# Kernel optimization log

Hardware: AMD Instinct MI355X
Metric: run time of the kernel (lower is better)

## Reference

```python
import jax, jax.numpy as jnp
import numpy as np

NUM_HEAD = 8
HEAD_DIM = 32
MAX_DIST = 128
RATIO = 4  # smooth_embedding_ratio


def setup_inputs() -> dict:
    key = jax.random.key(0)
    ks = jax.random.split(key, 8)
    B, L, C = 4, 2048, 64
    H, D, md = NUM_HEAD, HEAD_DIM, MAX_DIST
    Wsm = (2 * md + 1) // RATIO  # 64

    def g(k, shape, scale=0.05):
        return jax.random.normal(k, shape, dtype=jnp.float32) * scale

    return {
        "x": g(ks[0], (B, L, C), 1.0),
        "Wq": g(ks[1], (C, H * D)),
        "bq": jnp.zeros((H * D,), jnp.float32),
        "Wk": g(ks[2], (C, H * D)),
        "bk": jnp.zeros((H * D,), jnp.float32),
        "Wv": g(ks[3], (C, H)),
        "distance_pe": g(ks[4], (H, D, Wsm, 1)),
        "u_pe": g(ks[5], (H, 1, 1, D)),
        "v_pe": g(ks[6], (H, 1, 1, D)),
    }


def reference(x, Wq, bq, Wk, bk, Wv, distance_pe, u_pe, v_pe):
    H, D, md = NUM_HEAD, HEAD_DIM, MAX_DIST
    W = 2 * md + 1
    B, L, _ = x.shape

    # projections, split into heads: (H, B, L, D)
    q = (x @ Wq + bq).reshape(B, L, H, D).transpose(2, 0, 1, 3)
    k = (x @ Wk + bk).reshape(B, L, H, D).transpose(2, 0, 1, 3)
    v = jax.nn.sigmoid(x @ Wv).transpose(2, 0, 1)  # (H, B, L)

    # Banded (q+u) @ k^T without materializing the full LxL score matrix.
    # TF does matmul + diag_part(k=(-md, md)) + permute + double reverse, which
    # equals att[h,b,n,m] = <q_u[h,b,(L-1-n)-(m-md)], k[h,b,L-1-n]> (0 if OOB).
    q_u = q + u_pe  # (H, B, L, D)
    q_pad = jnp.pad(q_u, ((0, 0), (0, 0), (md, md), (0, 0)))  # zeros match diag_part padding

    def band_at(m):
        # q_pad[j + 2*md - m] == q_u[j - (m - md)] (zero when out of range)
        qs = jax.lax.dynamic_slice_in_dim(q_pad, 2 * md - m, L, axis=2)
        return jnp.einsum('hbld,hbld->hbl', qs, k)

    band = jax.lax.map(band_at, jnp.arange(W))  # (W, H, B, L)
    att = jnp.transpose(band, (1, 2, 3, 0))[:, :, ::-1, :]  # (H, B, L, W)

    # Smoothed distance PE: bilinear upsample width Wsm -> W (TF2 half-pixel centers)
    smooth_pe = jax.image.resize(distance_pe, (H, D, W, 1), method='linear')[..., 0]  # (H, D, W)
    att = att + jnp.einsum('hbld,hdw->hblw', q + v_pe, smooth_pe)

    att = jax.nn.softmax(att * (float(D) ** -0.5), axis=-1)
    att = att * v[..., None]  # sigmoid value gating

    out = att.sum(axis=2)  # global mode: reduce over data_length -> (H, B, W)
    return jnp.transpose(out, (1, 2, 0))  # (B, W, H)
```

## Files before the change

kernel.cpp:

```cpp
#include <hip/hip_runtime.h>
#include <math.h>

#define NH 8
#define HD 32
#define MD 128
#define NW 257
#define NWP 272
#define WSM 64
#define NB 4
#define NL 2048
#define NC 64
#define NHD 256
#define SP 40
#define ROWS 128
#define WIN 384
#define SC2 0.2550928063161107f

#define PM_BLK 512
#define VV_BLK 64
#define SPE_BLK 34
#define WTS 72

using bf16x8 = __attribute__((ext_vector_type(8))) short;
using f32x4  = __attribute__((ext_vector_type(4))) float;
using i32x4  = __attribute__((ext_vector_type(4))) int;

__device__ __forceinline__ unsigned cvtpk(float lo, float hi) {
  unsigned r;
  asm("v_cvt_pk_bf16_f32 %0, %1, %2" : "=v"(r) : "v"(lo), "v"(hi));
  return r;
}
__device__ __forceinline__ void stb(unsigned short* p, float f) {
  *p = (unsigned short)cvtpk(f, f);
}

__global__ __launch_bounds__(256, 4) void projmm_kernel(
    const float* __restrict__ x,
    const float* __restrict__ Wq, const float* __restrict__ bq,
    const float* __restrict__ Wk, const float* __restrict__ bk,
    const float* __restrict__ Wv, const float* __restrict__ dpe,
    const float* __restrict__ u_pe, const float* __restrict__ v_pe,
    unsigned short* __restrict__ qu, unsigned short* __restrict__ qv,
    unsigned short* __restrict__ kb, float* __restrict__ vv,
    unsigned short* __restrict__ spt, float* __restrict__ out) {
  __shared__ __align__(16) unsigned short wt[128 * WTS];
  const int t = threadIdx.x;
  const int bid = blockIdx.x;

  if (bid >= PM_BLK + VV_BLK) {
    const int base = (bid - PM_BLK - VV_BLK) * 256 + t;
    if (base < NB * NW * NH) out[base] = 0.f;
    for (int idx = base; idx < NH * NWP * HD; idx += SPE_BLK * 256) {
      const int d = idx & 31;
      const int hm = idx >> 5;
      const int m = hm % NWP;
      const int h = hm / NWP;
      float val = 0.f;
      if (m < NW) {
        float tt = (m + 0.5f) * ((float)WSM / (float)NW) - 0.5f;
        tt = fminf(fmaxf(tt, 0.f), (float)(WSM - 1));
        const int i0 = (int)tt;
        const float f = tt - (float)i0;
        const int i1 = (i0 + 1 < WSM) ? i0 + 1 : WSM - 1;
        const float* bse = dpe + ((size_t)h * HD + d) * WSM;
        val = (bse[i0] * (1.f - f) + bse[i1] * f) * SC2;
      }
      stb(spt + idx, val);
    }
    return;
  }

  if (bid >= PM_BLK) {
    const int row = (bid - PM_BLK) * 128 + (t >> 1);
    const int h0 = (t & 1) * 4;
    const float* xr = x + (size_t)row * NC;
    float a0 = 0.f, a1 = 0.f, a2 = 0.f, a3 = 0.f;
#pragma unroll
    for (int c4 = 0; c4 < NC / 4; ++c4) {
      const float4 xv = *reinterpret_cast<const float4*>(xr + 4 * c4);
#pragma unroll
      for (int j = 0; j < 4; ++j) {
        const float xs = j == 0 ? xv.x : j == 1 ? xv.y : j == 2 ? xv.z : xv.w;
        const float4 wv = *reinterpret_cast<const float4*>(Wv + (4 * c4 + j) * NH + h0);
        a0 = fmaf(xs, wv.x, a0);
        a1 = fmaf(xs, wv.y, a1);
        a2 = fmaf(xs, wv.z, a2);
        a3 = fmaf(xs, wv.w, a3);
      }
    }
    const int b = row >> 11, ll = row & (NL - 1);
    vv[((size_t)(h0 + 0) * NB + b) * NL + ll] = 1.f / (1.f + __expf(-a0));
    vv[((size_t)(h0 + 1) * NB + b) * NL + ll] = 1.f / (1.f + __expf(-a1));
    vv[((size_t)(h0 + 2) * NB + b) * NL + ll] = 1.f / (1.f + __expf(-a2));
    vv[((size_t)(h0 + 3) * NB + b) * NL + ll] = 1.f / (1.f + __expf(-a3));
    return;
  }

  const int l64 = t & 63, w = t >> 6;
  const int c = l64 & 15, g = l64 >> 4, g8 = g * 8;
  const int br = bid >> 2;
  const int c0 = (bid & 3) << 7;
  const int r0 = br << 6;
  const int b = r0 >> 11;
  const int l0 = r0 & (NL - 1);

  const bool isQ = (c0 < 256);
  const float* Wsrc = isQ ? Wq : Wk;
  const int cb = isQ ? c0 : c0 - 256;

#pragma unroll
  for (int i = 0; i < 4; ++i) {
    const int flat = t + i * 256;
    const int col4 = flat & 31;
    const int kp = flat >> 5;
    const float4 w0 = *reinterpret_cast<const float4*>(Wsrc + (2 * kp) * NHD + cb + 4 * col4);
    const float4 w1 = *reinterpret_cast<const float4*>(Wsrc + (2 * kp + 1) * NHD + cb + 4 * col4);
    unsigned* wp = reinterpret_cast<unsigned*>(wt);
    wp[(4 * col4 + 0) * (WTS / 2) + kp] = cvtpk(w0.x, w1.x);
    wp[(4 * col4 + 1) * (WTS / 2) + kp] = cvtpk(w0.y, w1.y);
    wp[(4 * col4 + 2) * (WTS / 2) + kp] = cvtpk(w0.z, w1.z);
    wp[(4 * col4 + 3) * (WTS / 2) + kp] = cvtpk(w0.w, w1.w);
  }

  const float* xr = x + (size_t)(r0 + 16 * w + c) * NC;
  const float4 x00 = *reinterpret_cast<const float4*>(xr + g8);
  const float4 x01 = *reinterpret_cast<const float4*>(xr + g8 + 4);
  const float4 x10 = *reinterpret_cast<const float4*>(xr + 32 + g8);
  const float4 x11 = *reinterpret_cast<const float4*>(xr + 32 + g8 + 4);
  const i32x4 a0i = {(int)cvtpk(x00.x, x00.y), (int)cvtpk(x00.z, x00.w),
                     (int)cvtpk(x01.x, x01.y), (int)cvtpk(x01.z, x01.w)};
  const i32x4 a1i = {(int)cvtpk(x10.x, x10.y), (int)cvtpk(x10.z, x10.w),
                     (int)cvtpk(x11.x, x11.y), (int)cvtpk(x11.z, x11.w)};
  const bf16x8 a0 = __builtin_bit_cast(bf16x8, a0i);
  const bf16x8 a1 = __builtin_bit_cast(bf16x8, a1i);

  __syncthreads();

  f32x4 acc[8];
#pragma unroll
  for (int tt = 0; tt < 8; ++tt) acc[tt] = {0.f, 0.f, 0.f, 0.f};

#pragma unroll
  for (int tt = 0; tt < 8; ++tt) {
    const bf16x8 b0 = *reinterpret_cast<const bf16x8*>(&wt[(16 * tt + c) * WTS + g8]);
    const bf16x8 b1 = *reinterpret_cast<const bf16x8*>(&wt[(16 * tt + c) * WTS + 32 + g8]);
    acc[tt] = __builtin_amdgcn_mfma_f32_16x16x32_bf16(a0, b0, acc[tt], 0, 0, 0);
    acc[tt] = __builtin_amdgcn_mfma_f32_16x16x32_bf16(a1, b1, acc[tt], 0, 0, 0);
  }

#pragma unroll
  for (int tt = 0; tt < 8; ++tt) {
    const int col = cb + 16 * tt + c;
    const int h = col >> 5, d = col & 31;
    const size_t rowbase = (((size_t)h * NB + b) * NL + l0 + 16 * w) * HD + d;
    if (isQ) {
      const float bias = bq[col];
      const float uu = u_pe[col], vp = v_pe[col];
#pragma unroll
      for (int r = 0; r < 4; ++r) {
        const float val = acc[tt][r] + bias;
        stb(qu + rowbase + (size_t)(4 * g + r) * HD, val + uu);
        stb(qv + rowbase + (size_t)(4 * g + r) * HD, val + vp);
      }
    } else {
      const float bias = bk[col];
#pragma unroll
      for (int r = 0; r < 4; ++r)
        stb(kb + rowbase + (size_t)(4 * g + r) * HD, (acc[tt][r] + bias) * SC2);
    }
  }
}

__global__ __launch_bounds__(512, 4) void band_attn_mfma(
    const unsigned short* __restrict__ qu, const unsigned short* __restrict__ qv,
    const unsigned short* __restrict__ kb, const float* __restrict__ vv,
    const unsigned short* __restrict__ spt, float* __restrict__ out) {
  __shared__ __align__(16) unsigned short qu_sh[WIN * SP];
  float* red = reinterpret_cast<float*>(qu_sh);

  const int bid = blockIdx.x;
  const int tile = bid & 15;
  const int hb = bid >> 4;
  const int b = hb & (NB - 1);
  const int h = hb >> 2;
  const int n0 = tile << 7;
  const int jlo = NL - ROWS - n0;
  const int tid = threadIdx.x;
  const int l = tid & 63;
  const int w = tid >> 6;
  const int c = l & 15;
  const int g = l >> 4;
  const int g8 = g * 8;

  const unsigned short* qu_h = qu + (size_t)hb * NL * HD;
  const unsigned short* qv_h = qv + (size_t)hb * NL * HD;
  const unsigned short* k_h  = kb + (size_t)hb * NL * HD;
  const unsigned short* sp_h = spt + (size_t)h * NWP * HD;
  const float* vv_h = vv + (size_t)hb * NL;

  const bf16x8 ak  = *reinterpret_cast<const bf16x8*>(k_h  + (size_t)(jlo + 16 * w + c) * HD + g8);
  const bf16x8 aqv = *reinterpret_cast<const bf16x8*>(qv_h + (size_t)(n0 + 127 - 16 * w - c) * HD + g8);
  const f32x4 v4 = *reinterpret_cast<const f32x4*>(vv_h + (n0 + 124 - 16 * w - 4 * g));

  const int wq0_blk = jlo - MD;
  i32x4 stq[3];
#pragma unroll
  for (int it = 0; it < 3; ++it) {
    const int p = tid + it * 512;
    const int gr = wq0_blk + (p >> 2);
    i32x4 val = {0, 0, 0, 0};
    if ((unsigned)gr < (unsigned)NL)
      val = *reinterpret_cast<const i32x4*>(qu_h + (size_t)gr * HD + (p & 3) * 8);
    stq[it] = val;
  }

  const f32x4 z4 = {0.f, 0.f, 0.f, 0.f};

  f32x4 s[17];
#pragma unroll
  for (int t = 0; t < 17; ++t) {
    const bf16x8 bsp = *reinterpret_cast<const bf16x8*>(sp_h + (size_t)(16 * t + c) * HD + g8);
    s[t] = __builtin_amdgcn_mfma_f32_16x16x32_bf16(aqv, bsp, z4, 0, 0, 0);
  }

#pragma unroll
  for (int it = 0; it < 3; ++it) {
    const int p = tid + it * 512;
    *reinterpret_cast<i32x4*>(&qu_sh[(p >> 2) * SP + (p & 3) * 8]) = stq[it];
  }
  __syncthreads();

  int sl[4]; bool cond[4];
#pragma unroll
  for (int r = 0; r < 4; ++r) {
    sl[r] = 16 * g + ((4 * g + r - c) & 15);
    cond[r] = (4 * g + r) >= c;
  }

  f32x4 shp;
#pragma unroll
  for (int U = 0; U <= 16; ++U) {
    const bf16x8 bqu = *reinterpret_cast<const bf16x8*>(&qu_sh[(16 * w + 16 * U + c) * SP + g8]);
    const f32x4 c1 = __builtin_amdgcn_mfma_f32_16x16x32_bf16(ak, bqu, z4, 0, 0, 0);

    f32x4 shc;
#pragma unroll
    for (int r = 0; r < 4; ++r) shc[r] = __shfl(c1[r], sl[r], 64);

    if (U == 0) {
#pragma unroll
      for (int r = 0; r < 4; ++r)
        s[16][r] = (c == 0) ? (s[16][r] + shc[r]) : -1e30f;
    } else {
#pragma unroll
      for (int r = 0; r < 4; ++r)
        s[16 - U][r] += cond[r] ? shc[r] : shp[r];
    }
    shp = shc;
  }

  float wgt[4];
#pragma unroll
  for (int r = 0; r < 4; ++r) {
    float sum = 0.f;
#pragma unroll
    for (int t = 0; t < 17; ++t) {
      const float p = exp2f(s[t][r]);
      s[t][r] = p;
      sum += p;
    }
#pragma unroll
    for (int off = 1; off < 16; off <<= 1) sum += __shfl_xor(sum, off, 16);
    wgt[r] = v4[3 - r] * __builtin_amdgcn_rcpf(sum);
  }

  __syncthreads();
#pragma unroll
  for (int t = 0; t < 17; ++t) {
    float y = s[t][0] * wgt[0] + s[t][1] * wgt[1] + s[t][2] * wgt[2] + s[t][3] * wgt[3];
    y += __shfl_xor(y, 16, 64);
    y += __shfl_xor(y, 32, 64);
    if (l < 16) red[w * NWP + 16 * t + c] = y;
  }
  __syncthreads();
  for (int m = tid; m < NW; m += 512) {
    float ssum = 0.f;
#pragma unroll
    for (int ww = 0; ww < 8; ++ww) ssum += red[ww * NWP + m];
    atomicAdd(&out[((size_t)b * NW + m) * NH + h], ssum);
  }
}

extern "C" void kernel_launch(void* const* d_in, const int* in_sizes, int n_in,
                              void* d_out, int out_size, void* d_ws, size_t ws_size,
                              hipStream_t stream) {
  const float* x = (const float*)d_in[0];
  const float* Wq = (const float*)d_in[1];
  const float* bq = (const float*)d_in[2];
  const float* Wk = (const float*)d_in[3];
  const float* bk = (const float*)d_in[4];
  const float* Wv = (const float*)d_in[5];
  const float* dpe = (const float*)d_in[6];
  const float* u_pe = (const float*)d_in[7];
  const float* v_pe = (const float*)d_in[8];
  float* out = (float*)d_out;

  const size_t qk_elems = (size_t)NH * NB * NL * HD;
  float* vv = (float*)d_ws;
  unsigned short* qu = (unsigned short*)(vv + (size_t)NH * NB * NL);
  unsigned short* qv = qu + qk_elems;
  unsigned short* kb = qv + qk_elems;
  unsigned short* spt = kb + qk_elems;

  hipLaunchKernelGGL(projmm_kernel, dim3(PM_BLK + VV_BLK + SPE_BLK), dim3(256), 0, stream,
                     x, Wq, bq, Wk, bk, Wv, dpe, u_pe, v_pe, qu, qv, kb, vv, spt, out);
  hipLaunchKernelGGL(band_attn_mfma, dim3(NH * NB * (NL / ROWS)), dim3(512), 0, stream,
                     qu, qv, kb, vv, spt, out);
}
```

Baseline: 33.86 us.

## Fuse projection and band attention into one cooperative kernel with grid sync

Merges the projection kernel and the band-attention kernel into a single cooperative launch of 512 blocks of 512 threads, with a grid-wide sync between the phases. The sigmoid-gate and smoothed-PE work move onto spare thread ranges inside the 512 projection blocks instead of running in separate blocks. The goal is to remove the second launch and the kernel-boundary gap. In exchange it adds per-call occupancy and attribute queries on the host, depends on all 512 blocks being co-resident, and keeps a two-kernel fallback.

```diff
diff --git a/kernel.cpp b/kernel.cpp
--- a/kernel.cpp
+++ b/kernel.cpp
@@ -1,5 +1,8 @@
 #include <hip/hip_runtime.h>
+#include <hip/hip_cooperative_groups.h>
 #include <math.h>
+
+namespace cg = cooperative_groups;
 
 #define NH 8
 #define HD 32
@@ -14,12 +17,10 @@
 #define SP 40
 #define ROWS 128
 #define WIN 384
+#define WTS 72
 #define SC2 0.2550928063161107f
 
-#define PM_BLK 512
-#define VV_BLK 64
-#define SPE_BLK 34
-#define WTS 72
+#define NBLK 512
 
 using bf16x8 = __attribute__((ext_vector_type(8))) short;
 using f32x4  = __attribute__((ext_vector_type(4))) float;
@@ -34,7 +35,8 @@
   *p = (unsigned short)cvtpk(f, f);
 }
 
-__global__ __launch_bounds__(256, 4) void projmm_kernel(
+__device__ __forceinline__ void phaseA_body(
+    unsigned short* wt, int bid, int tid,
     const float* __restrict__ x,
     const float* __restrict__ Wq, const float* __restrict__ bq,
     const float* __restrict__ Wk, const float* __restrict__ bk,
@@ -43,149 +45,145 @@
     unsigned short* __restrict__ qu, unsigned short* __restrict__ qv,
     unsigned short* __restrict__ kb, float* __restrict__ vv,
     unsigned short* __restrict__ spt, float* __restrict__ out) {
-  __shared__ __align__(16) unsigned short wt[128 * WTS];
-  const int t = threadIdx.x;
-  const int bid = blockIdx.x;
-
-  if (bid >= PM_BLK + VV_BLK) {
-    const int base = (bid - PM_BLK - VV_BLK) * 256 + t;
-    if (base < NB * NW * NH) out[base] = 0.f;
-    for (int idx = base; idx < NH * NWP * HD; idx += SPE_BLK * 256) {
-      const int d = idx & 31;
-      const int hm = idx >> 5;
-      const int m = hm % NWP;
-      const int h = hm / NWP;
-      float val = 0.f;
-      if (m < NW) {
-        float tt = (m + 0.5f) * ((float)WSM / (float)NW) - 0.5f;
-        tt = fminf(fmaxf(tt, 0.f), (float)(WSM - 1));
-        const int i0 = (int)tt;
-        const float f = tt - (float)i0;
-        const int i1 = (i0 + 1 < WSM) ? i0 + 1 : WSM - 1;
-        const float* bse = dpe + ((size_t)h * HD + d) * WSM;
-        val = (bse[i0] * (1.f - f) + bse[i1] * f) * SC2;
-      }
-      stb(spt + idx, val);
-    }
-    return;
-  }
-
-  if (bid >= PM_BLK) {
-    const int row = (bid - PM_BLK) * 128 + (t >> 1);
-    const int h0 = (t & 1) * 4;
+  bf16x8 a0, a1;
+  int c = 0, g = 0, g8 = 0, w = 0, b = 0, l0 = 0, cb = 0;
+  bool isQ = true;
+
+  if (tid < 256) {
+    const int t = tid;
+    const int l64 = t & 63;
+    w = t >> 6;
+    c = l64 & 15; g = l64 >> 4; g8 = g * 8;
+    const int br = bid >> 2;
+    const int c0 = (bid & 3) << 7;
+    const int r0 = br << 6;
+    b = r0 >> 11;
+    l0 = r0 & (NL - 1);
+    isQ = (c0 < 256);
+    const float* Wsrc = isQ ? Wq : Wk;
+    cb = isQ ? c0 : c0 - 256;
+
+#pragma unroll
+    for (int i = 0; i < 4; ++i) {
+      const int flat = t + i * 256;
+      const int col4 = flat & 31;
+      const int kp = flat >> 5;
+      const float4 w0 = *reinterpret_cast<const float4*>(Wsrc + (2 * kp) * NHD + cb + 4 * col4);
+      const float4 w1 = *reinterpret_cast<const float4*>(Wsrc + (2 * kp + 1) * NHD + cb + 4 * col4);
+      unsigned* wp = reinterpret_cast<unsigned*>(wt);
+      wp[(4 * col4 + 0) * (WTS / 2) + kp] = cvtpk(w0.x, w1.x);
+      wp[(4 * col4 + 1) * (WTS / 2) + kp] = cvtpk(w0.y, w1.y);
+      wp[(4 * col4 + 2) * (WTS / 2) + kp] = cvtpk(w0.z, w1.z);
+      wp[(4 * col4 + 3) * (WTS / 2) + kp] = cvtpk(w0.w, w1.w);
+    }
+
+    const float* xr = x + (size_t)(r0 + 16 * w + c) * NC;
+    const float4 x00 = *reinterpret_cast<const float4*>(xr + g8);
+    const float4 x01 = *reinterpret_cast<const float4*>(xr + g8 + 4);
+    const float4 x10 = *reinterpret_cast<const float4*>(xr + 32 + g8);
+    const float4 x11 = *reinterpret_cast<const float4*>(xr + 32 + g8 + 4);
+    const i32x4 a0i = {(int)cvtpk(x00.x, x00.y), (int)cvtpk(x00.z, x00.w),
+                       (int)cvtpk(x01.x, x01.y), (int)cvtpk(x01.z, x01.w)};
+    const i32x4 a1i = {(int)cvtpk(x10.x, x10.y), (int)cvtpk(x10.z, x10.w),
+                       (int)cvtpk(x11.x, x11.y), (int)cvtpk(x11.z, x11.w)};
+    a0 = __builtin_bit_cast(bf16x8, a0i);
+    a1 = __builtin_bit_cast(bf16x8, a1i);
+  } else if (tid < 384) {
+    const int k = tid - 256;
+    const int j = k >> 3, hh = k & 7;
+    const int row = bid * 16 + j;
     const float* xr = x + (size_t)row * NC;
-    float a0 = 0.f, a1 = 0.f, a2 = 0.f, a3 = 0.f;
+    float a = 0.f;
 #pragma unroll
     for (int c4 = 0; c4 < NC / 4; ++c4) {
       const float4 xv = *reinterpret_cast<const float4*>(xr + 4 * c4);
-#pragma unroll
-      for (int j = 0; j < 4; ++j) {
-        const float xs = j == 0 ? xv.x : j == 1 ? xv.y : j == 2 ? xv.z : xv.w;
-        const float4 wv = *reinterpret_cast<const float4*>(Wv + (4 * c4 + j) * NH + h0);
-        a0 = fmaf(xs, wv.x, a0);
-        a1 = fmaf(xs, wv.y, a1);
-        a2 = fmaf(xs, wv.z, a2);
-        a3 = fmaf(xs, wv.w, a3);
+      a = fmaf(xv.x, Wv[(4 * c4 + 0) * NH + hh], a);
+      a = fmaf(xv.y, Wv[(4 * c4 + 1) * NH + hh], a);
+      a = fmaf(xv.z, Wv[(4 * c4 + 2) * NH + hh], a);
+      a = fmaf(xv.w, Wv[(4 * c4 + 3) * NH + hh], a);
+    }
+    const int bb = row >> 11, ll = row & (NL - 1);
+    vv[((size_t)hh * NB + bb) * NL + ll] = 1.f / (1.f + __expf(-a));
+  } else {
+    const int k = tid - 384;
+    if (k < 17) {
+      const int oz = bid * 17 + k;
+      if (oz < NB * NW * NH) out[oz] = 0.f;
+    }
+#pragma unroll
+    for (int it = 0; it < 2; ++it) {
+      const int k2 = k + it * 128;
+      const int idx = bid * 136 + k2;
+      if (k2 < 136 && idx < NH * NWP * HD) {
+        const int d = idx & 31;
+        const int hm = idx >> 5;
+        const int m = hm % NWP;
+        const int h = hm / NWP;
+        float val = 0.f;
+        if (m < NW) {
+          float tt = (m + 0.5f) * ((float)WSM / (float)NW) - 0.5f;
+          tt = fminf(fmaxf(tt, 0.f), (float)(WSM - 1));
+          const int i0 = (int)tt;
+          const float f = tt - (float)i0;
+          const int i1 = (i0 + 1 < WSM) ? i0 + 1 : WSM - 1;
+          const float* bse = dpe + ((size_t)h * HD + d) * WSM;
+          val = (bse[i0] * (1.f - f) + bse[i1] * f) * SC2;
+        }
+        stb(spt + idx, val);
       }
     }
-    const int b = row >> 11, ll = row & (NL - 1);
-    vv[((size_t)(h0 + 0) * NB + b) * NL + ll] = 1.f / (1.f + __expf(-a0));
-    vv[((size_t)(h0 + 1) * NB + b) * NL + ll] = 1.f / (1.f + __expf(-a1));
-    vv[((size_t)(h0 + 2) * NB + b) * NL + ll] = 1.f / (1.f + __expf(-a2));
-    vv[((size_t)(h0 + 3) * NB + b) * NL + ll] = 1.f / (1.f + __expf(-a3));
-    return;
-  }
-
-  const int l64 = t & 63, w = t >> 6;
-  const int c = l64 & 15, g = l64 >> 4, g8 = g * 8;
-  const int br = bid >> 2;
-  const int c0 = (bid & 3) << 7;
-  const int r0 = br << 6;
-  const int b = r0 >> 11;
-  const int l0 = r0 & (NL - 1);
-
-  const bool isQ = (c0 < 256);
-  const float* Wsrc = isQ ? Wq : Wk;
-  const int cb = isQ ? c0 : c0 - 256;
-
-#pragma unroll
-  for (int i = 0; i < 4; ++i) {
-    const int flat = t + i * 256;
-    const int col4 = flat & 31;
-    const int kp = flat >> 5;
-    const float4 w0 = *reinterpret_cast<const float4*>(Wsrc + (2 * kp) * NHD + cb + 4 * col4);
-    const float4 w1 = *reinterpret_cast<const float4*>(Wsrc + (2 * kp + 1) * NHD + cb + 4 * col4);
-    unsigned* wp = reinterpret_cast<unsigned*>(wt);
-    wp[(4 * col4 + 0) * (WTS / 2) + kp] = cvtpk(w0.x, w1.x);
-    wp[(4 * col4 + 1) * (WTS / 2) + kp] = cvtpk(w0.y, w1.y);
-    wp[(4 * col4 + 2) * (WTS / 2) + kp] = cvtpk(w0.z, w1.z);
-    wp[(4 * col4 + 3) * (WTS / 2) + kp] = cvtpk(w0.w, w1.w);
-  }
-
-  const float* xr = x + (size_t)(r0 + 16 * w + c) * NC;
-  const float4 x00 = *reinterpret_cast<const float4*>(xr + g8);
-  const float4 x01 = *reinterpret_cast<const float4*>(xr + g8 + 4);
-  const float4 x10 = *reinterpret_cast<const float4*>(xr + 32 + g8);
-  const float4 x11 = *reinterpret_cast<const float4*>(xr + 32 + g8 + 4);
-  const i32x4 a0i = {(int)cvtpk(x00.x, x00.y), (int)cvtpk(x00.z, x00.w),
-                     (int)cvtpk(x01.x, x01.y), (int)cvtpk(x01.z, x01.w)};
-  const i32x4 a1i = {(int)cvtpk(x10.x, x10.y), (int)cvtpk(x10.z, x10.w),
-                     (int)cvtpk(x11.x, x11.y), (int)cvtpk(x11.z, x11.w)};
-  const bf16x8 a0 = __builtin_bit_cast(bf16x8, a0i);
-  const bf16x8 a1 = __builtin_bit_cast(bf16x8, a1i);
+  }
 
   __syncthreads();
 
-  f32x4 acc[8];
-#pragma unroll
-  for (int tt = 0; tt < 8; ++tt) acc[tt] = {0.f, 0.f, 0.f, 0.f};
-
-#pragma unroll
-  for (int tt = 0; tt < 8; ++tt) {
-    const bf16x8 b0 = *reinterpret_cast<const bf16x8*>(&wt[(16 * tt + c) * WTS + g8]);
-    const bf16x8 b1 = *reinterpret_cast<const bf16x8*>(&wt[(16 * tt + c) * WTS + 32 + g8]);
-    acc[tt] = __builtin_amdgcn_mfma_f32_16x16x32_bf16(a0, b0, acc[tt], 0, 0, 0);
-    acc[tt] = __builtin_amdgcn_mfma_f32_16x16x32_bf16(a1, b1, acc[tt], 0, 0, 0);
-  }
-
-#pragma unroll
-  for (int tt = 0; tt < 8; ++tt) {
-    const int col = cb + 16 * tt + c;
-    const int h = col >> 5, d = col & 31;
-    const size_t rowbase = (((size_t)h * NB + b) * NL + l0 + 16 * w) * HD + d;
-    if (isQ) {
-      const float bias = bq[col];
-      const float uu = u_pe[col], vp = v_pe[col];
-#pragma unroll
-      for (int r = 0; r < 4; ++r) {
-        const float val = acc[tt][r] + bias;
-        stb(qu + rowbase + (size_t)(4 * g + r) * HD, val + uu);
-        stb(qv + rowbase + (size_t)(4 * g + r) * HD, val + vp);
+  if (tid < 256) {
+    f32x4 acc[8];
+#pragma unroll
+    for (int tt = 0; tt < 8; ++tt) acc[tt] = {0.f, 0.f, 0.f, 0.f};
+#pragma unroll
+    for (int tt = 0; tt < 8; ++tt) {
+      const bf16x8 b0 = *reinterpret_cast<const bf16x8*>(&wt[(16 * tt + c) * WTS + g8]);
+      const bf16x8 b1 = *reinterpret_cast<const bf16x8*>(&wt[(16 * tt + c) * WTS + 32 + g8]);
+      acc[tt] = __builtin_amdgcn_mfma_f32_16x16x32_bf16(a0, b0, acc[tt], 0, 0, 0);
+      acc[tt] = __builtin_amdgcn_mfma_f32_16x16x32_bf16(a1, b1, acc[tt], 0, 0, 0);
+    }
+#pragma unroll
+    for (int tt = 0; tt < 8; ++tt) {
+      const int col = cb + 16 * tt + c;
+      const int h = col >> 5, d = col & 31;
+      const size_t rowbase = (((size_t)h * NB + b) * NL + l0 + 16 * w) * HD + d;
+      if (isQ) {
+        const float bias = bq[col];
+        const float uu = u_pe[col], vp = v_pe[col];
+#pragma unroll
+        for (int r = 0; r < 4; ++r) {
+          const float val = acc[tt][r] + bias;
+          stb(qu + rowbase + (size_t)(4 * g + r) * HD, val + uu);
+          stb(qv + rowbase + (size_t)(4 * g + r) * HD, val + vp);
+        }
+      } else {
+        const float bias = bk[col];
+#pragma unroll
+        for (int r = 0; r < 4; ++r)
+          stb(kb + rowbase + (size_t)(4 * g + r) * HD, (acc[tt][r] + bias) * SC2);
       }
-    } else {
-      const float bias = bk[col];
-#pragma unroll
-      for (int r = 0; r < 4; ++r)
-        stb(kb + rowbase + (size_t)(4 * g + r) * HD, (acc[tt][r] + bias) * SC2);
-    }
-  }
-}
-
-__global__ __launch_bounds__(512, 4) void band_attn_mfma(
+    }
+  }
+}
+
+__device__ __forceinline__ void phaseB_body(
+    unsigned short* qu_sh, int bid, int tid,
     const unsigned short* __restrict__ qu, const unsigned short* __restrict__ qv,
     const unsigned short* __restrict__ kb, const float* __restrict__ vv,
     const unsigned short* __restrict__ spt, float* __restrict__ out) {
-  __shared__ __align__(16) unsigned short qu_sh[WIN * SP];
   float* red = reinterpret_cast<float*>(qu_sh);
 
-  const int bid = blockIdx.x;
   const int tile = bid & 15;
   const int hb = bid >> 4;
   const int b = hb & (NB - 1);
   const int h = hb >> 2;
   const int n0 = tile << 7;
   const int jlo = NL - ROWS - n0;
-  const int tid = threadIdx.x;
   const int l = tid & 63;
   const int w = tid >> 6;
   const int c = l & 15;
@@ -242,11 +240,9 @@
   for (int U = 0; U <= 16; ++U) {
     const bf16x8 bqu = *reinterpret_cast<const bf16x8*>(&qu_sh[(16 * w + 16 * U + c) * SP + g8]);
     const f32x4 c1 = __builtin_amdgcn_mfma_f32_16x16x32_bf16(ak, bqu, z4, 0, 0, 0);
-
     f32x4 shc;
 #pragma unroll
     for (int r = 0; r < 4; ++r) shc[r] = __shfl(c1[r], sl[r], 64);
-
     if (U == 0) {
 #pragma unroll
       for (int r = 0; r < 4; ++r)
@@ -289,6 +285,45 @@
     for (int ww = 0; ww < 8; ++ww) ssum += red[ww * NWP + m];
     atomicAdd(&out[((size_t)b * NW + m) * NH + h], ssum);
   }
+}
+
+__global__ __launch_bounds__(512, 4) void fused_coop(
+    const float* __restrict__ x,
+    const float* __restrict__ Wq, const float* __restrict__ bq,
+    const float* __restrict__ Wk, const float* __restrict__ bk,
+    const float* __restrict__ Wv, const float* __restrict__ dpe,
+    const float* __restrict__ u_pe, const float* __restrict__ v_pe,
+    unsigned short* __restrict__ qu, unsigned short* __restrict__ qv,
+    unsigned short* __restrict__ kb, float* __restrict__ vv,
+    unsigned short* __restrict__ spt, float* __restrict__ out) {
+  __shared__ __align__(16) unsigned short smem[WIN * SP];
+  phaseA_body(smem, blockIdx.x, threadIdx.x, x, Wq, bq, Wk, bk, Wv, dpe, u_pe, v_pe,
+              qu, qv, kb, vv, spt, out);
+  __threadfence();
+  cg::this_grid().sync();
+  phaseB_body(smem, blockIdx.x, threadIdx.x, qu, qv, kb, vv, spt, out);
+}
+
+__global__ __launch_bounds__(512, 4) void phaseA_kernel(
+    const float* __restrict__ x,
+    const float* __restrict__ Wq, const float* __restrict__ bq,
+    const float* __restrict__ Wk, const float* __restrict__ bk,
+    const float* __restrict__ Wv, const float* __restrict__ dpe,
+    const float* __restrict__ u_pe, const float* __restrict__ v_pe,
+    unsigned short* __restrict__ qu, unsigned short* __restrict__ qv,
+    unsigned short* __restrict__ kb, float* __restrict__ vv,
+    unsigned short* __restrict__ spt, float* __restrict__ out) {
+  __shared__ __align__(16) unsigned short smem[128 * WTS];
+  phaseA_body(smem, blockIdx.x, threadIdx.x, x, Wq, bq, Wk, bk, Wv, dpe, u_pe, v_pe,
+              qu, qv, kb, vv, spt, out);
+}
+
+__global__ __launch_bounds__(512, 4) void phaseB_kernel(
+    const unsigned short* __restrict__ qu, const unsigned short* __restrict__ qv,
+    const unsigned short* __restrict__ kb, const float* __restrict__ vv,
+    const unsigned short* __restrict__ spt, float* __restrict__ out) {
+  __shared__ __align__(16) unsigned short smem[WIN * SP];
+  phaseB_body(smem, blockIdx.x, threadIdx.x, qu, qv, kb, vv, spt, out);
 }
 
 extern "C" void kernel_launch(void* const* d_in, const int* in_sizes, int n_in,
@@ -312,8 +347,23 @@
   unsigned short* kb = qv + qk_elems;
   unsigned short* spt = kb + qk_elems;
 
-  hipLaunchKernelGGL(projmm_kernel, dim3(PM_BLK + VV_BLK + SPE_BLK), dim3(256), 0, stream,
+  int coopAttr = 0, numCU = 0, maxPerCU = 0;
+  hipDeviceGetAttribute(&coopAttr, hipDeviceAttributeCooperativeLaunch, 0);
+  hipDeviceGetAttribute(&numCU, hipDeviceAttributeMultiprocessorCount, 0);
+  hipOccupancyMaxActiveBlocksPerMultiprocessor(&maxPerCU, (const void*)fused_coop, 512, 0);
+
+  if (coopAttr && maxPerCU > 0 && (long)maxPerCU * numCU >= NBLK) {
+    void* args[] = {(void*)&x, (void*)&Wq, (void*)&bq, (void*)&Wk, (void*)&bk,
+                    (void*)&Wv, (void*)&dpe, (void*)&u_pe, (void*)&v_pe,
+                    (void*)&qu, (void*)&qv, (void*)&kb, (void*)&vv, (void*)&spt,
+                    (void*)&out};
+    if (hipLaunchCooperativeKernel((const void*)fused_coop, dim3(NBLK), dim3(512),
+                                   args, 0, stream) == hipSuccess)
+      return;
+  }
+
+  hipLaunchKernelGGL(phaseA_kernel, dim3(NBLK), dim3(512), 0, stream,
                      x, Wq, bq, Wk, bk, Wv, dpe, u_pe, v_pe, qu, qv, kb, vv, spt, out);
-  hipLaunchKernelGGL(band_attn_mfma, dim3(NH * NB * (NL / ROWS)), dim3(512), 0, stream,
+  hipLaunchKernelGGL(phaseB_kernel, dim3(NBLK), dim3(512), 0, stream,
                      qu, qv, kb, vv, spt, out);
 }
```

Result: no change. 34.14 us (+0.8%).
